# Kernel tuning notes

Measured on AMD Instinct MI355X. Metric: run time of the kernel, lower is better.

Reference implementation:

```python
import jax, jax.numpy as jnp
import numpy as np

ICM2IFS = 2.99792458e-05
KB = 0.6950389


def _forward(T, Er, cortim, dt, psi0, Hfull, W1, b1, W2, b2, W3, b3, W4, b4,
             save_interval, remat=False):
    # Faithful vectorized translation of MLNISE.forward with T_correction='ML',
    # explicitTemp='None', saveCoherence=False, saveU=False. The original
    # nested (ii, jj) Python loops are fully independent across (ii, jj), so
    # they are vectorized into one [B, N, N] pass per timestep.
    B, Tp1, N, _ = Hfull.shape
    kBT = T * KB                                             # [B]
    factor = (1j * 2.0 * np.pi * ICM2IFS) * dt.astype(jnp.complex64)  # [B]
    E0, C0 = jnp.linalg.eigh(Hfull[:, 0])
    phiB0 = jnp.einsum('bji,bjk->bik', C0.astype(jnp.complex64),
                       psi0.astype(jnp.complex64))           # Cold^T @ psi0
    jidx = jnp.arange(N)[None, :, None]

    def mlp(x):
        h = jax.nn.elu(x @ W1.T + b1)
        h = jax.nn.elu(h @ W2.T + b2)
        h = jax.nn.elu(h @ W3.T + b3)
        return jax.nn.elu(h @ W4.T + b4)

    def step(carry, Ht):
        Cold, Eold, phiB = carry
        E, C = jnp.linalg.eigh(Ht)
        S = jnp.einsum('bja,bjc->bac', C, Cold)              # S[b, jj, ii] = (C^T Cold)
        kk = jnp.argmax(S * S, axis=1)                       # [B, N] max over jj per ii
        is_kk = jidx == kk[:, None, :]                       # [B, N(jj), N(ii)]
        DE = jnp.where(is_kk, 0.0, E[:, :, None] - Eold[:, None, :])
        phi2 = jnp.real(phiB[:, :, 0]) ** 2 + jnp.imag(phiB[:, :, 0]) ** 2  # [B, N]
        p_ii = phi2[:, None, :]
        p_jj = phi2[:, :, None]
        m = p_ii > 0.01 * p_jj
        ratio = jnp.where(m, p_jj / jnp.where(m, p_ii, 1.0), 100.0)
        kbt = kBT[:, None, None]
        ones = jnp.ones_like(S)
        feat = jnp.stack([DE, ratio, S, kbt * ones,
                          Er[:, None, None] * ones, cortim[:, None, None] * ones,
                          jnp.zeros_like(S), jnp.exp(DE / kbt)], axis=-1)  # [B,N,N,8]
        corr = (mlp(feat.reshape(B * N * N, 8)) + 1.0).reshape(B, N, N)
        S2 = S * corr
        CD = jnp.sum(jnp.where(is_kk, 0.0, S2 * S2), axis=1)  # [B, N] per ii
        S_kk = jnp.take_along_axis(S2, kk[:, None, :], axis=1)[:, 0, :]  # [B, N]
        nrm = jnp.abs(S_kk)
        nrm = jnp.where(nrm > 0, nrm, 1.0)
        pos = (1.0 - CD) > 0
        newval = jnp.where(pos, jnp.sqrt(jnp.clip(1.0 - CD, 0.0)) * S_kk / nrm, S_kk)
        S2 = jnp.where(is_kk, newval[:, None, :], S2)
        phase = jnp.exp(-E.astype(jnp.complex64) * factor[:, None])  # [B, N]
        U = phase[:, :, None] * S2.astype(jnp.complex64)      # diag(phase) @ S
        phiB = U @ phiB
        phiB = phiB / jnp.sqrt(jnp.sum(jnp.real(phiB) ** 2 + jnp.imag(phiB) ** 2,
                                       axis=1, keepdims=True))
        ploc = jnp.einsum('bij,bjk->bik', C.astype(jnp.complex64), phiB)
        ps = jnp.real(ploc[:, :, 0]) ** 2 + jnp.imag(ploc[:, :, 0]) ** 2
        return (C, E, phiB), ps

    f = jax.checkpoint(step) if remat else step
    Hts = jnp.moveaxis(Hfull[:, 1:], 1, 0)                   # time-major [steps,B,N,N]
    _, ps_all = jax.lax.scan(f, (C0, E0, phiB0), Hts)
    saved = jnp.moveaxis(ps_all[save_interval - 1::save_interval], 0, 1)
    return jnp.concatenate([(psi0[:, :, 0] ** 2)[:, None, :], saved], axis=1)


def setup_inputs() -> dict:
    key = jax.random.key(0)
    ks = jax.random.split(key, 8)
    B, N, steps, SI = 32, 32, 600, 10
    A = 50.0 * jax.random.normal(ks[0], (B, steps + 1, N, N), dtype=jnp.float32)
    Hfull = 0.5 * (A + jnp.swapaxes(A, -1, -2))              # symmetric per snapshot
    psi0 = jnp.zeros((B, N, 1), jnp.float32).at[:, 0, 0].set(1.0)
    T = 250.0 + 100.0 * jax.random.uniform(ks[1], (B,), jnp.float32)
    Er = 1.0 + 35.0 * jax.random.uniform(ks[2], (B,), jnp.float32)
    cortim = 10.0 + 100.0 * jax.random.uniform(ks[3], (B,), jnp.float32)
    dt = jnp.ones((B,), jnp.float32)
    total_time = jnp.full((B,), float(steps), jnp.float32)
    reps = jnp.arange(B, dtype=jnp.int32)

    def lin(k, fo, fi):
        kw, kb = jax.random.split(k)
        bnd = 1.0 / np.sqrt(fi)
        W = jax.random.uniform(kw, (fo, fi), jnp.float32, -bnd, bnd) / 10.0
        b = jax.random.uniform(kb, (fo,), jnp.float32, -bnd, bnd)
        return W, b

    W1, b1 = lin(ks[4], 75, 8)
    W2, b2 = lin(ks[5], 75, 75)
    W3, b3 = lin(ks[6], 75, 75)
    W4, b4 = lin(ks[7], 1, 75)
    return dict(T=T, Er=Er, cortim=cortim, total_time=total_time, dt=dt, reps=reps,
                psi0=psi0, Hfull=Hfull, W1=W1, b1=b1, W2=W2, b2=b2, W3=W3, b3=b3,
                W4=W4, b4=b4, save_interval=SI)


def reference(T, Er, cortim, total_time, dt, reps, psi0, Hfull,
              W1, b1, W2, b2, W3, b3, W4, b4, save_interval):
    # total_time/dt only set the (static) number of steps = Hfull.shape[1]-1;
    # reps only sets the batch size. Both are encoded in the array shapes.
    return _forward(T, Er, cortim, dt, psi0, Hfull,
                    W1, b1, W2, b2, W3, b3, W4, b4, save_interval)
```

## Files before the change

### kernel.cpp

```cpp
#include <hip/hip_runtime.h>
#include <math.h>


#define NB 32
#define NN 32
#define NSTEPS 600
#define NT1 601
#define NSI 10
#define NH 75
#define NU 80
#define NKB 20
#define NIB 8

#define ICM2IFS 2.99792458e-05
#define KBOLTZ 0.6950389f
#define TWO_PI 6.283185307179586476925286766559

__device__ __forceinline__ float elu1(float x) { return x > 0.f ? x : (__expf(x) - 1.f); }

__global__ __launch_bounds__(128) void eigh_kernel(const float* __restrict__ Hf,
                                                   float* __restrict__ E_all,
                                                   float* __restrict__ CT_all)
{
    __shared__ double A[NN][NN + 1];
    __shared__ float  V[NN][NN + 1];
    __shared__ double csC[16], csS[16];
    __shared__ int   prC[16], qrC[16];
    __shared__ double redv;
    __shared__ int   rankl[NN];

    const int idx = blockIdx.x;
    const int tid = threadIdx.x;
    const float* Hp = Hf + (size_t)idx * (NN * NN);

    for (int e = tid; e < NN * NN; e += 128) {
        A[e >> 5][e & 31] = (double)Hp[e];
        V[e >> 5][e & 31] = ((e >> 5) == (e & 31)) ? 1.f : 0.f;
    }
    __syncthreads();

    if (tid < 64) {
        double part = 0.0;
        for (int e = tid; e < NN * NN; e += 64) { double v = A[e >> 5][e & 31]; part += v * v; }
        #pragma unroll
        for (int off = 32; off > 0; off >>= 1) part += __shfl_down(part, off);
        if (tid == 0) redv = part;
    }
    __syncthreads();
    const double tol2 = 1e-20 * redv;

    for (int sweep = 0; sweep < 10; ++sweep) {
        for (int r = 0; r < NN - 1; ++r) {
            if (tid < 16) {
                int m = tid, p, q;
                if (m == 0) { p = 0; q = 1 + (r % 31); }
                else { p = 1 + ((m + r) % 31); q = 1 + ((31 - m + r) % 31); }
                double apq = A[p][q];
                double c = 1.0, sn = 0.0;
                if (apq != 0.0) {
                    double theta = 0.5 * (A[q][q] - A[p][p]) / apq;
                    double tt = 1.0 / (fabs(theta) + sqrt(theta * theta + 1.0));
                    if (theta < 0.0) tt = -tt;
                    c = 1.0 / sqrt(tt * tt + 1.0);
                    sn = tt * c;
                }
                csC[m] = c; csS[m] = sn; prC[m] = p; qrC[m] = q;
            }
            __syncthreads();
            #pragma unroll
            for (int it = 0; it < 4; ++it) {
                int task = tid + it * 128;
                int m = task >> 5, jc = task & 31;
                int p = prC[m], q = qrC[m];
                double c = csC[m], sn = csS[m];
                double ap = A[p][jc], aq = A[q][jc];
                A[p][jc] = c * ap - sn * aq;
                A[q][jc] = sn * ap + c * aq;
            }
            __syncthreads();
            #pragma unroll
            for (int it = 0; it < 8; ++it) {
                int task = tid + it * 128;
                int m = (task >> 5) & 15, ir = task & 31;
                int p = prC[m], q = qrC[m];
                if (task < 512) {
                    double c = csC[m], sn = csS[m];
                    double aip = A[ir][p], aiq = A[ir][q];
                    A[ir][p] = c * aip - sn * aiq;
                    A[ir][q] = sn * aip + c * aiq;
                } else {
                    float cf = (float)csC[m], sf = (float)csS[m];
                    float vip = V[ir][p], viq = V[ir][q];
                    V[ir][p] = cf * vip - sf * viq;
                    V[ir][q] = sf * vip + cf * viq;
                }
            }
            __syncthreads();
        }
        if (sweep >= 3) {
            if (tid < 64) {
                double o = 0.0;
                for (int e = tid; e < NN * NN; e += 64) {
                    int i2 = e >> 5, j2 = e & 31;
                    double v = A[i2][j2];
                    o += (i2 != j2) ? v * v : 0.0;
                }
                #pragma unroll
                for (int off = 32; off > 0; off >>= 1) o += __shfl_down(o, off);
                if (tid == 0) redv = o;
            }
            __syncthreads();
            if (redv <= tol2) break;
        }
    }
    __syncthreads();

    if (tid < NN) {
        double ei = A[tid][tid];
        int rk = 0;
        for (int j2 = 0; j2 < NN; ++j2) {
            double ej = A[j2][j2];
            rk += (ej < ei || (ej == ei && j2 < tid)) ? 1 : 0;
        }
        rankl[tid] = rk;
        E_all[(size_t)idx * NN + rk] = (float)ei;
    }
    __syncthreads();
    float* ct = CT_all + (size_t)idx * NN * NN;
    for (int e = tid; e < NN * NN; e += 128) {
        int col = e >> 5, m2 = e & 31;
        ct[(size_t)rankl[col] * NN + m2] = V[m2][col];
    }
}

__global__ __launch_bounds__(256) void kk_kernel(const float* __restrict__ CT_all,
                                                 int* __restrict__ kk_all)
{
    __shared__ float Ct[NN][NN + 1], Cp[NN][NN + 1], S[NN][NN + 1];
    const int blk = blockIdx.x;
    const int b = blk / NSTEPS, s = blk % NSTEPS + 1;
    const int tid = threadIdx.x;
    const float* ctg = CT_all + ((size_t)b * NT1 + s) * (NN * NN);
    const float* cpg = CT_all + ((size_t)b * NT1 + s - 1) * (NN * NN);
    for (int e = tid; e < NN * NN; e += 256) {
        Ct[e >> 5][e & 31] = ctg[e];
        Cp[e >> 5][e & 31] = cpg[e];
    }
    __syncthreads();
    for (int e = tid; e < NN * NN; e += 256) {
        int i = e >> 5, j = e & 31;
        float acc = 0.f;
        for (int m = 0; m < NN; ++m) acc += Ct[i][m] * Cp[j][m];
        S[i][j] = acc;
    }
    __syncthreads();
    if (tid < NN) {
        const int j = tid;
        float best = -1.f; int bi = 0;
        for (int i = 0; i < NN; ++i) {
            float v = S[i][j]; v *= v;
            if (v > best) { best = v; bi = i; }
        }
        kk_all[(size_t)blk * NN + j] = bi;
    }
}

__global__ void wtrans_kernel(const float* __restrict__ W1, const float* __restrict__ b1,
                              const float* __restrict__ W2, const float* __restrict__ W3,
                              const float* __restrict__ b2, const float* __restrict__ b3,
                              const float* __restrict__ W4,
                              float* __restrict__ W2p, float* __restrict__ W3p,
                              float4* __restrict__ L1W4, float4* __restrict__ L1B4,
                              float* __restrict__ bpad)
{
    const int tid = threadIdx.x;
    const int tot = 8 * NKB * 4 * 12;
    for (int e = tid; e < tot; e += 256) {
        int ug = e / (NKB * 4 * 12);
        int kb = (e / (4 * 12)) % NKB;
        int kp = (e / 12) & 3;
        int uu = e % 12;
        int u = ug * 10 + uu;
        int k = kb * 4 + kp;
        float v2 = 0.f, v3 = 0.f;
        if (uu < 10 && u < NH && k < NH) {
            v2 = W2[u * NH + k];
            v3 = W3[u * NH + k];
        }
        W2p[e] = v2; W3p[e] = v3;
    }
    if (tid < NU) {
        if (tid < NH) {
            const float* w = W1 + tid * 8;
            L1W4[tid] = make_float4(w[0], w[1], w[2], w[7]);
            L1B4[tid] = make_float4(w[3], w[4], w[5], b1[tid]);
            bpad[tid]          = b2[tid];
            bpad[NU + tid]     = b3[tid];
            bpad[2 * NU + tid] = W4[tid];
        } else {
            L1W4[tid] = make_float4(0.f, 0.f, 0.f, 0.f);
            L1B4[tid] = make_float4(0.f, 0.f, 0.f, 0.f);
            bpad[tid] = 0.f; bpad[NU + tid] = 0.f; bpad[2 * NU + tid] = 0.f;
        }
    }
}

__global__ __launch_bounds__(512, 2) void persist_kernel(
    const float* __restrict__ E_all, const float* __restrict__ CT_all,
    const int* __restrict__ kk_all, const float* __restrict__ psi0,
    const float* __restrict__ Tarr, const float* __restrict__ ErA,
    const float* __restrict__ ctA, const float* __restrict__ dtA,
    const float* __restrict__ W2p, const float* __restrict__ W3p,
    const float4* __restrict__ L1W4g, const float4* __restrict__ L1B4g,
    const float* __restrict__ bpad, const float* __restrict__ b4v,
    double* __restrict__ part_g, unsigned int* __restrict__ cnt,
    float* __restrict__ out)
{
    extern __shared__ __align__(16) float dyn[];
    float4* L1Wl = (float4*)dyn;
    float4* L1Bl = L1Wl + NU;
    float* cst  = (float*)(L1Bl + NU);
    float* b2l  = cst + NU;
    float* b3l  = b2l + NU;
    float* W4l  = b3l + NU;
    float* hbuf = W4l + NU;

    __shared__ float CpN[2][NN][NN + 4];
    __shared__ float4 featS[128];
    __shared__ float2 a4b2[8][64];
    __shared__ float EL[2][NN];
    __shared__ int   kkL[2][NN];
    __shared__ double phre[NN], phim[NN];
    __shared__ double ppre[4][NN], ppim[4][NN];
    __shared__ double sre[NN], sim[NN];
    __shared__ float phi2l[NN];

    const int tid  = threadIdx.x;
    const int b    = blockIdx.x >> 3;
    const int iblk = blockIdx.x & 7;
    const int j0   = iblk * 4;
    const int ug   = __builtin_amdgcn_readfirstlane(tid >> 6);
    const int rg   = tid & 63;
    const int U    = ug * 10;

    const float kbt = KBOLTZ * Tarr[b];
    const float er  = ErA[b];
    const float cti = ctA[b];
    const double dtb = (double)dtA[b];
    const float b4s = b4v[0];

    const float4* W2g = (const float4*)(W2p + (size_t)ug * (NKB * 48));
    const float4* W3g = (const float4*)(W3p + (size_t)ug * (NKB * 48));

    if (tid < NU) {
        L1Wl[tid] = L1W4g[tid];
        L1Bl[tid] = L1B4g[tid];
        b2l[tid] = bpad[tid];
        b3l[tid] = bpad[NU + tid];
        W4l[tid] = bpad[2 * NU + tid];
    }
    __syncthreads();
    if (tid < NU) {
        float4 lb = L1Bl[tid];
        cst[tid] = lb.w + lb.x * kbt + lb.y * er + lb.z * cti;
    }

    {
        const float* c0g = CT_all + (size_t)b * NT1 * NN * NN;
        const float* c1g = c0g + NN * NN;
        for (int e = tid; e < NN * NN; e += 512) {
            CpN[0][e >> 5][e & 31] = c0g[e];
            CpN[1][e >> 5][e & 31] = c1g[e];
        }
        if (tid < NN) {
            EL[0][tid] = E_all[((size_t)b * NT1 + 0) * NN + tid];
            EL[1][tid] = E_all[((size_t)b * NT1 + 1) * NN + tid];
            kkL[1][tid] = kk_all[(size_t)b * NSTEPS * NN + tid];
        }
        __syncthreads();
        if (tid < NN) {
            const int i = tid;
            double acc = 0.0;
            for (int j = 0; j < NN; ++j) acc += (double)CpN[0][i][j] * (double)psi0[b * NN + j];
            phre[i] = acc; phim[i] = 0.0;
            phi2l[i] = (float)(acc * acc);
            if (iblk == 0) {
                float p0 = psi0[b * NN + i];
                out[((size_t)b * 61) * NN + i] = p0 * p0;
            }
        }
        __syncthreads();
        {
            const int r = tid >> 2, c = tid & 3;
            const int i = r & 31, j = j0 + (r >> 5);
            float Sv = 0.f;
            #pragma unroll
            for (int m = c; m < NN; m += 4)
                Sv += CpN[1][i][m] * CpN[0][j][m];
            Sv += __shfl_xor(Sv, 1); Sv += __shfl_xor(Sv, 2);
            if (c == 0) {
                const int kj = kkL[1][j];
                const float DE = (i == kj) ? 0.f : (EL[1][i] - EL[0][j]);
                featS[r] = make_float4(DE, 100.f, Sv, __expf(DE / kbt));
            }
        }
        __syncthreads();
        if (tid < 128) {
            const int i = tid & 31, j = j0 + (tid >> 5);
            const float p_i = phi2l[i], p_j = phi2l[j];
            featS[tid].y = (p_j > 0.01f * p_i) ? (p_i / p_j) : 100.f;
        }
    }

    for (int t = 1; t <= NSTEPS; ++t) {
        __syncthreads();
        const int cur = t & 1;

        float2 cpre = make_float2(0.f, 0.f);
        float  epre = 0.f;
        int    kpre = 0;
        if (t < NSTEPS) {
            const float* c1g = CT_all + ((size_t)b * NT1 + t + 1) * (NN * NN);
            cpre = ((const float2*)c1g)[tid];
            if (tid < NN) epre = E_all[((size_t)b * NT1 + t + 1) * NN + tid];
            else if (tid < 2 * NN) kpre = kk_all[((size_t)b * NSTEPS + t) * NN + (tid - NN)];
        }

        {
            float4 f0 = featS[2 * rg], f1 = featS[2 * rg + 1];
            #pragma unroll
            for (int u = 0; u < 10; ++u) {
                float4 wv = L1Wl[U + u];
                float c = cst[U + u];
                float2 hv;
                hv.x = elu1(c + wv.x * f0.x + wv.y * f0.y + wv.z * f0.z + wv.w * f0.w);
                hv.y = elu1(c + wv.x * f1.x + wv.y * f1.y + wv.z * f1.z + wv.w * f1.w);
                *(float2*)(hbuf + (U + u) * 128 + 2 * rg) = hv;
            }
        }
        __syncthreads();

        float2 acc[10];
        #pragma unroll
        for (int u = 0; u < 10; ++u) { float bb = b2l[U + u]; acc[u] = make_float2(bb, bb); }
        for (int kb = 0; kb < NKB; ++kb) {
            float4 wv[12];
            float2 hv[4];
            #pragma unroll
            for (int m = 0; m < 12; ++m) wv[m] = W2g[kb * 12 + m];
            #pragma unroll
            for (int kk = 0; kk < 4; ++kk)
                hv[kk] = *(const float2*)(hbuf + (kb * 4 + kk) * 128 + 2 * rg);
            #pragma unroll
            for (int kk = 0; kk < 4; ++kk) {
                const float* wf = (const float*)&wv[kk * 3];
                #pragma unroll
                for (int u = 0; u < 10; ++u) {
                    float wS = wf[u];
                    acc[u].x += wS * hv[kk].x; acc[u].y += wS * hv[kk].y;
                }
            }
        }
        __syncthreads();
        #pragma unroll
        for (int u = 0; u < 10; ++u) {
            float2 hv; hv.x = elu1(acc[u].x); hv.y = elu1(acc[u].y);
            *(float2*)(hbuf + (U + u) * 128 + 2 * rg) = hv;
        }
        __syncthreads();

        #pragma unroll
        for (int u = 0; u < 10; ++u) { float bb = b3l[U + u]; acc[u] = make_float2(bb, bb); }
        for (int kb = 0; kb < NKB; ++kb) {
            float4 wv[12];
            float2 hv[4];
            #pragma unroll
            for (int m = 0; m < 12; ++m) wv[m] = W3g[kb * 12 + m];
            #pragma unroll
            for (int kk = 0; kk < 4; ++kk)
                hv[kk] = *(const float2*)(hbuf + (kb * 4 + kk) * 128 + 2 * rg);
            #pragma unroll
            for (int kk = 0; kk < 4; ++kk) {
                const float* wf = (const float*)&wv[kk * 3];
                #pragma unroll
                for (int u = 0; u < 10; ++u) {
                    float wS = wf[u];
                    acc[u].x += wS * hv[kk].x; acc[u].y += wS * hv[kk].y;
                }
            }
        }
        {
            float2 p4 = make_float2(0.f, 0.f);
            #pragma unroll
            for (int u = 0; u < 10; ++u) {
                float w4 = W4l[U + u];
                p4.x += w4 * elu1(acc[u].x); p4.y += w4 * elu1(acc[u].y);
            }
            a4b2[ug][rg] = p4;
        }
        __syncthreads();

        if (tid < 128) {
            const int r = tid;
            const int i = r & 31;
            const int jj = r >> 5;
            const int j = j0 + jj;
            float a4 = b4s;
            #pragma unroll
            for (int g = 0; g < 8; ++g) {
                float2 pv = a4b2[g][r >> 1];
                a4 += (r & 1) ? pv.y : pv.x;
            }
            const float corr = elu1(a4) + 1.f;
            float s2v = featS[r].z * corr;
            const int kj = kkL[cur][j];
            double v = (double)s2v;
            double cd = (i == kj) ? 0.0 : v * v;
            cd += __shfl_xor(cd, 1);  cd += __shfl_xor(cd, 2);
            cd += __shfl_xor(cd, 4);  cd += __shfl_xor(cd, 8);
            cd += __shfl_xor(cd, 16);
            if (i == kj) {
                double nrm = fabs(v); nrm = (nrm > 0.0) ? nrm : 1.0;
                double rem = 1.0 - cd;
                v = (rem > 0.0) ? (sqrt(rem) * v / nrm) : v;
                v = (double)(float)v;
            }
            ppre[jj][i] = v * phre[j];
            ppim[jj][i] = v * phim[j];
        }

        if (t < NSTEPS) {
            const int e0 = tid * 2;
            CpN[1 - cur][e0 >> 5][e0 & 31] = cpre.x;
            CpN[1 - cur][e0 >> 5][(e0 & 31) + 1] = cpre.y;
            if (tid < NN) EL[1 - cur][tid] = epre;
            else if (tid < 2 * NN) kkL[1 - cur][tid - NN] = kpre;
        }
        __syncthreads();

        if (tid < 32) {
            const int i = tid;
            double pr = ((ppre[0][i] + ppre[1][i]) + ppre[2][i]) + ppre[3][i];
            double pi = ((ppim[0][i] + ppim[1][i]) + ppim[2][i]) + ppim[3][i];
            double* pg = part_g + ((size_t)cur * NB + b) * 512;
            __hip_atomic_store(&pg[i * 8 + iblk], pr,
                               __ATOMIC_RELAXED, __HIP_MEMORY_SCOPE_AGENT);
            __hip_atomic_store(&pg[256 + i * 8 + iblk], pi,
                               __ATOMIC_RELAXED, __HIP_MEMORY_SCOPE_AGENT);
            asm volatile("s_waitcnt vmcnt(0)" ::: "memory");
            if (tid == 0)
                __hip_atomic_fetch_add(cnt + (size_t)b * NSTEPS + (t - 1), 1u,
                                       __ATOMIC_RELAXED, __HIP_MEMORY_SCOPE_AGENT);
        }

        if (t < NSTEPS) {
            const int curS = 1 - cur;
            const int r = tid >> 2, c = tid & 3;
            const int i = r & 31, j = j0 + (r >> 5);
            float Sv = 0.f;
            #pragma unroll
            for (int m = c; m < NN; m += 4)
                Sv += CpN[curS][i][m] * CpN[1 - curS][j][m];
            Sv += __shfl_xor(Sv, 1); Sv += __shfl_xor(Sv, 2);
            if (c == 0) {
                const int kj = kkL[curS][j];
                const float DE = (i == kj) ? 0.f : (EL[curS][i] - EL[1 - curS][j]);
                featS[r] = make_float4(DE, 100.f, Sv, __expf(DE / kbt));
            }
        }

        if (tid == 0) {
            const unsigned int* c = cnt + (size_t)b * NSTEPS + (t - 1);
            while (__hip_atomic_load(c, __ATOMIC_RELAXED, __HIP_MEMORY_SCOPE_AGENT)
                   < (unsigned)NIB) {
                __builtin_amdgcn_s_sleep(2);
            }
        }
        __syncthreads();

        {
            const double* pg = part_g + ((size_t)cur * NB + b) * 512;
            double v = __hip_atomic_load(&pg[tid], __ATOMIC_RELAXED,
                                         __HIP_MEMORY_SCOPE_AGENT);
            v += __shfl_xor(v, 1); v += __shfl_xor(v, 2); v += __shfl_xor(v, 4);
            if ((tid & 7) == 0) {
                const int i = (tid >> 3) & 31;
                if (tid < 256) sre[i] = v; else sim[i] = v;
            }
        }
        __syncthreads();

        if (tid < NN) {
            const int ii = tid;
            double are = sre[ii], aim = sim[ii];
            double th = (double)EL[cur][ii] * (TWO_PI * ICM2IFS) * dtb;
            double x2 = th * th;
            double sph = th * (1.0 + x2 * (-1.0 / 6.0 + x2 * (1.0 / 120.0 + x2 * (-1.0 / 5040.0 + x2 * (1.0 / 362880.0)))));
            double cph = 1.0 + x2 * (-0.5 + x2 * (1.0 / 24.0 + x2 * (-1.0 / 720.0 + x2 * (1.0 / 40320.0))));
            double nre = cph * are + sph * aim;
            double nim = cph * aim - sph * are;
            double v = nre * nre + nim * nim;
            double s = v;
            s += __shfl_xor(s, 1); s += __shfl_xor(s, 2); s += __shfl_xor(s, 4);
            s += __shfl_xor(s, 8); s += __shfl_xor(s, 16);
            double sc = 1.0 / sqrt(s);
            double nr = nre * sc, ni = nim * sc;
            phre[ii] = nr; phim[ii] = ni;
            phi2l[ii] = (float)(nr * nr + ni * ni);
        }
        __syncthreads();

        if ((t % NSI) == 0 && tid < 64) {
            const int ii = iblk * 4 + (tid >> 4), l = tid & 15;
            double are = 0.0, aim = 0.0;
            #pragma unroll
            for (int jj = l; jj < NN; jj += 16) {
                double cij = (double)CpN[cur][jj][ii];
                are += cij * phre[jj]; aim += cij * phim[jj];
            }
            are += __shfl_xor(are, 1); aim += __shfl_xor(aim, 1);
            are += __shfl_xor(are, 2); aim += __shfl_xor(aim, 2);
            are += __shfl_xor(are, 4); aim += __shfl_xor(aim, 4);
            are += __shfl_xor(are, 8); aim += __shfl_xor(aim, 8);
            if (l == 0)
                out[((size_t)b * 61 + t / NSI) * NN + ii] = (float)(are * are + aim * aim);
        }
        if (t < NSTEPS && tid < 128) {
            const int i = tid & 31, j = j0 + (tid >> 5);
            const float p_i = phi2l[i], p_j = phi2l[j];
            featS[tid].y = (p_j > 0.01f * p_i) ? (p_i / p_j) : 100.f;
        }
    }
}

extern "C" void kernel_launch(void* const* d_in, const int* in_sizes, int n_in,
                              void* d_out, int out_size, void* d_ws, size_t ws_size,
                              hipStream_t stream)
{
    const float* Tarr = (const float*)d_in[0];
    const float* ErA  = (const float*)d_in[1];
    const float* ctA  = (const float*)d_in[2];
    const float* dtA  = (const float*)d_in[4];
    const float* psi0 = (const float*)d_in[6];
    const float* Hf   = (const float*)d_in[7];
    const float* W1   = (const float*)d_in[8];
    const float* b1   = (const float*)d_in[9];
    const float* W2   = (const float*)d_in[10];
    const float* b2   = (const float*)d_in[11];
    const float* W3   = (const float*)d_in[12];
    const float* b3   = (const float*)d_in[13];
    const float* W4   = (const float*)d_in[14];
    const float* b4   = (const float*)d_in[15];

    unsigned int* cnt = (unsigned int*)d_ws;
    float* E_all  = (float*)(cnt + (size_t)NB * NSTEPS);
    float* CT_all = E_all + (size_t)NB * NT1 * NN;
    float* W2p    = CT_all + (size_t)NB * NT1 * NN * NN;
    float* W3p    = W2p + 8 * NKB * 48;
    float4* L1W4  = (float4*)(W3p + 8 * NKB * 48);
    float4* L1B4  = L1W4 + NU;
    float* bpad   = (float*)(L1B4 + NU);
    double* part_g = (double*)(bpad + 3 * NU);
    int*   kk_all = (int*)(part_g + 2 * (size_t)NB * 512);
    float* outp   = (float*)d_out;

    hipMemsetAsync(cnt, 0, (size_t)NB * NSTEPS * sizeof(unsigned int), stream);
    eigh_kernel<<<NB * NT1, 128, 0, stream>>>(Hf, E_all, CT_all);
    wtrans_kernel<<<1, 256, 0, stream>>>(W1, b1, W2, W3, b2, b3, W4,
                                         W2p, W3p, L1W4, L1B4, bpad);
    kk_kernel<<<NB * NSTEPS, 256, 0, stream>>>(CT_all, kk_all);

    const size_t dynf = (size_t)(8 * NU) + 4 * NU + NU * 128;
    persist_kernel<<<NB * NIB, 512, dynf * sizeof(float), stream>>>(E_all, CT_all,
        kk_all, psi0, Tarr, ErA, ctA, dtA, W2p, W3p, L1W4, L1B4, bpad, b4,
        part_g, cnt, outp);
}
```

Baseline: 13.70 ms.

## Fuse per-step argmax overlap computation into persistent kernel, drop kk_kernel

Removes the separate kk_kernel, which recomputed every overlap matrix S just to find the per-column argmax. The persistent kernel already computes S, so it now finds the argmax with a warp-shuffle reduction that also breaks ties toward the lowest index. It then fills the DE and exp(DE/kbT) features in place. In the time loop this work runs on otherwise idle threads (256–383) alongside the phase/normalisation update, and it removes the global kk_all reads and writes. The cost is a little more work per step on the serial critical path of the persistent kernel.

```diff
diff --git a/kernel.cpp b/kernel.cpp
--- a/kernel.cpp
+++ b/kernel.cpp
@@ -130,38 +130,6 @@
     for (int e = tid; e < NN * NN; e += 128) {
         int col = e >> 5, m2 = e & 31;
         ct[(size_t)rankl[col] * NN + m2] = V[m2][col];
-    }
-}
-
-__global__ __launch_bounds__(256) void kk_kernel(const float* __restrict__ CT_all,
-                                                 int* __restrict__ kk_all)
-{
-    __shared__ float Ct[NN][NN + 1], Cp[NN][NN + 1], S[NN][NN + 1];
-    const int blk = blockIdx.x;
-    const int b = blk / NSTEPS, s = blk % NSTEPS + 1;
-    const int tid = threadIdx.x;
-    const float* ctg = CT_all + ((size_t)b * NT1 + s) * (NN * NN);
-    const float* cpg = CT_all + ((size_t)b * NT1 + s - 1) * (NN * NN);
-    for (int e = tid; e < NN * NN; e += 256) {
-        Ct[e >> 5][e & 31] = ctg[e];
-        Cp[e >> 5][e & 31] = cpg[e];
-    }
-    __syncthreads();
-    for (int e = tid; e < NN * NN; e += 256) {
-        int i = e >> 5, j = e & 31;
-        float acc = 0.f;
-        for (int m = 0; m < NN; ++m) acc += Ct[i][m] * Cp[j][m];
-        S[i][j] = acc;
-    }
-    __syncthreads();
-    if (tid < NN) {
-        const int j = tid;
-        float best = -1.f; int bi = 0;
-        for (int i = 0; i < NN; ++i) {
-            float v = S[i][j]; v *= v;
-            if (v > best) { best = v; bi = i; }
-        }
-        kk_all[(size_t)blk * NN + j] = bi;
     }
 }
 
@@ -207,7 +175,7 @@
 
 __global__ __launch_bounds__(512, 2) void persist_kernel(
     const float* __restrict__ E_all, const float* __restrict__ CT_all,
-    const int* __restrict__ kk_all, const float* __restrict__ psi0,
+    const float* __restrict__ psi0,
     const float* __restrict__ Tarr, const float* __restrict__ ErA,
     const float* __restrict__ ctA, const float* __restrict__ dtA,
     const float* __restrict__ W2p, const float* __restrict__ W3p,
@@ -275,7 +243,6 @@
         if (tid < NN) {
             EL[0][tid] = E_all[((size_t)b * NT1 + 0) * NN + tid];
             EL[1][tid] = E_all[((size_t)b * NT1 + 1) * NN + tid];
-            kkL[1][tid] = kk_all[(size_t)b * NSTEPS * NN + tid];
         }
         __syncthreads();
         if (tid < NN) {
@@ -298,17 +265,26 @@
             for (int m = c; m < NN; m += 4)
                 Sv += CpN[1][i][m] * CpN[0][j][m];
             Sv += __shfl_xor(Sv, 1); Sv += __shfl_xor(Sv, 2);
-            if (c == 0) {
-                const int kj = kkL[1][j];
-                const float DE = (i == kj) ? 0.f : (EL[1][i] - EL[0][j]);
-                featS[r] = make_float4(DE, 100.f, Sv, __expf(DE / kbt));
-            }
+            if (c == 0) featS[r] = make_float4(0.f, 0.f, Sv, 0.f);
         }
         __syncthreads();
         if (tid < 128) {
-            const int i = tid & 31, j = j0 + (tid >> 5);
+            const int r = tid, i = r & 31, jj = r >> 5;
+            const int j = j0 + jj;
+            const float Sv = featS[r].z;
+            float v2 = Sv * Sv;
+            int bi = i;
+            #pragma unroll
+            for (int off = 16; off > 0; off >>= 1) {
+                float ov = __shfl_xor(v2, off);
+                int   oi = __shfl_xor(bi, off);
+                if (ov > v2 || (ov == v2 && oi < bi)) { v2 = ov; bi = oi; }
+            }
+            if (i == 0) kkL[1][j] = bi;
+            const float DE = (i == bi) ? 0.f : (EL[1][i] - EL[0][j]);
             const float p_i = phi2l[i], p_j = phi2l[j];
-            featS[tid].y = (p_j > 0.01f * p_i) ? (p_i / p_j) : 100.f;
+            const float ratio = (p_j > 0.01f * p_i) ? (p_i / p_j) : 100.f;
+            featS[r] = make_float4(DE, ratio, Sv, __expf(DE / kbt));
         }
     }
 
@@ -318,12 +294,10 @@
 
         float2 cpre = make_float2(0.f, 0.f);
         float  epre = 0.f;
-        int    kpre = 0;
         if (t < NSTEPS) {
             const float* c1g = CT_all + ((size_t)b * NT1 + t + 1) * (NN * NN);
             cpre = ((const float2*)c1g)[tid];
             if (tid < NN) epre = E_all[((size_t)b * NT1 + t + 1) * NN + tid];
-            else if (tid < 2 * NN) kpre = kk_all[((size_t)b * NSTEPS + t) * NN + (tid - NN)];
         }
 
         {
@@ -434,7 +408,6 @@
             CpN[1 - cur][e0 >> 5][e0 & 31] = cpre.x;
             CpN[1 - cur][e0 >> 5][(e0 & 31) + 1] = cpre.y;
             if (tid < NN) EL[1 - cur][tid] = epre;
-            else if (tid < 2 * NN) kkL[1 - cur][tid - NN] = kpre;
         }
         __syncthreads();
 
@@ -462,11 +435,7 @@
             for (int m = c; m < NN; m += 4)
                 Sv += CpN[curS][i][m] * CpN[1 - curS][j][m];
             Sv += __shfl_xor(Sv, 1); Sv += __shfl_xor(Sv, 2);
-            if (c == 0) {
-                const int kj = kkL[curS][j];
-                const float DE = (i == kj) ? 0.f : (EL[curS][i] - EL[1 - curS][j]);
-                featS[r] = make_float4(DE, 100.f, Sv, __expf(DE / kbt));
-            }
+            if (c == 0) featS[r] = make_float4(0.f, 0.f, Sv, 0.f);
         }
 
         if (tid == 0) {
@@ -507,6 +476,24 @@
             double nr = nre * sc, ni = nim * sc;
             phre[ii] = nr; phim[ii] = ni;
             phi2l[ii] = (float)(nr * nr + ni * ni);
+        } else if (t < NSTEPS && tid >= 256 && tid < 384) {
+            const int r = tid - 256;
+            const int i = r & 31, jj = r >> 5;
+            const int j = j0 + jj;
+            const int curS = 1 - cur;
+            const float Sv = featS[r].z;
+            float v2 = Sv * Sv;
+            int bi = i;
+            #pragma unroll
+            for (int off = 16; off > 0; off >>= 1) {
+                float ov = __shfl_xor(v2, off);
+                int   oi = __shfl_xor(bi, off);
+                if (ov > v2 || (ov == v2 && oi < bi)) { v2 = ov; bi = oi; }
+            }
+            if (i == 0) kkL[curS][j] = bi;
+            const float DE = (i == bi) ? 0.f : (EL[curS][i] - EL[cur][j]);
+            featS[r].x = DE;
+            featS[r].w = __expf(DE / kbt);
         }
         __syncthreads();
 
@@ -561,17 +548,15 @@
     float4* L1B4  = L1W4 + NU;
     float* bpad   = (float*)(L1B4 + NU);
     double* part_g = (double*)(bpad + 3 * NU);
-    int*   kk_all = (int*)(part_g + 2 * (size_t)NB * 512);
     float* outp   = (float*)d_out;
 
     hipMemsetAsync(cnt, 0, (size_t)NB * NSTEPS * sizeof(unsigned int), stream);
     eigh_kernel<<<NB * NT1, 128, 0, stream>>>(Hf, E_all, CT_all);
     wtrans_kernel<<<1, 256, 0, stream>>>(W1, b1, W2, W3, b2, b3, W4,
                                          W2p, W3p, L1W4, L1B4, bpad);
-    kk_kernel<<<NB * NSTEPS, 256, 0, stream>>>(CT_all, kk_all);
 
     const size_t dynf = (size_t)(8 * NU) + 4 * NU + NU * 128;
     persist_kernel<<<NB * NIB, 512, dynf * sizeof(float), stream>>>(E_all, CT_all,
-        kk_all, psi0, Tarr, ErA, ctA, dtA, W2p, W3p, L1W4, L1B4, bpad, b4,
+        psi0, Tarr, ErA, ctA, dtA, W2p, W3p, L1W4, L1B4, bpad, b4,
         part_g, cnt, outp);
 }
```

Result: no change. 13.64 ms (-0.5%).
